# Kernel optimization log

Hardware: AMD Instinct MI355X
Metric: run time of the kernel (lower is better)

Reference implementation:

```python
import jax, jax.numpy as jnp
import numpy as np

B, D, M, P, I, O = 256, 10, 32, 36, 8, 16
NUM_ITERATIONS = 3
EPS = 1e-07


def squash(s, axis=-1):
    sq = jnp.sum(s * s, axis=axis, keepdims=True)
    safe_norm = jnp.sqrt(sq + EPS)
    scale = sq / (1.0 + sq)
    return scale * (s / safe_norm)


def setup_inputs() -> dict:
    key = jax.random.key(0)
    kx, kw = jax.random.split(key)
    x = jax.random.normal(kx, (B, M, P, I), dtype=jnp.float32)
    # Parameter shape matches torch: [1, D, M, 1, O, I]
    W = 0.01 * jax.random.normal(kw, (1, D, M, 1, O, I), dtype=jnp.float32)
    return {"x": x, "W": W}


def reference(x, W):
    Wd = W[0, :, :, 0]  # [D, M, O, I]
    # u_hat: [B, D, M, P, O]
    u_hat = jnp.einsum('dmoi,bmpi->bdmpo', Wd, x)
    tu = jax.lax.stop_gradient(u_hat)
    b = jnp.zeros(u_hat.shape[:4], dtype=u_hat.dtype)  # [B, D, M, P]
    for _ in range(NUM_ITERATIONS - 1):
        c = jax.nn.softmax(b, axis=1)                 # over digit caps
        s = jnp.einsum('bdmp,bdmpo->bdo', c, tu)
        v = squash(s)
        b = b + jnp.einsum('bdmpo,bdo->bdmp', tu, v)
    # Final softmax over dim=3 (primary-cap axis), faithful to source
    c = jax.nn.softmax(b, axis=3)
    s = jnp.einsum('bdmp,bdmpo->bdo', c, u_hat)
    return squash(s)
```

## Files before the change

kernel.cpp:

```cpp
#include <hip/hip_runtime.h>
#include <math.h>

#define BB 256
#define DD 10
#define MM 32
#define PP 36
#define II 8
#define OO 16
#define NT 320
#define XS 292
#define RS 37

__device__ __forceinline__ float dot8(const float4 a0, const float4 a1,
                                      const float4 b0, const float4 b1) {
    return a0.x*b0.x + a0.y*b0.y + a0.z*b0.z + a0.w*b0.w
         + a1.x*b1.x + a1.y*b1.y + a1.z*b1.z + a1.w*b1.w;
}
__device__ __forceinline__ float dot4(const float4 a, const float4 b) {
    return a.x*b.x + a.y*b.y + a.z*b.z + a.w*b.w;
}

__global__ void __launch_bounds__(NT, 3) caps_routing(
    const float* __restrict__ x,
    const float* __restrict__ W,
    float* __restrict__ out)
{
    const int bidx = blockIdx.x & 255;
    const int half = blockIdx.x >> 8;
    const int tid  = threadIdx.x;
    const int wave = tid >> 6;
    const int lane = tid & 63;
    const float* __restrict__ xb = x + (size_t)bidx * (MM*PP*II);

    __shared__ __align__(16) float xs  [MM*XS];
    __shared__ __align__(16) float z   [DD*MM*II];
    __shared__ __align__(16) float y   [5*MM*II];
    __shared__ __align__(16) float ybar[MM*II];
    __shared__ __align__(16) float rinv[MM*RS];

    {
        const float4* xg = (const float4*)xb;
        #pragma unroll
        for (int k = 0; k < 8; ++k) {
            const int t = tid + k*NT;
            if (t < MM*72) {
                const int m = t / 72, r = t - m*72;
                *(float4*)(xs + m*XS + 4*r) = xg[t];
            }
        }
        if (tid < MM*II) {
            const int m = tid >> 3, i = tid & 7;
            const float* xr = xb + m*(PP*II) + i;
            float acc = 0.f;
            #pragma unroll 6
            for (int p = 0; p < PP; ++p) acc += xr[p*II];
            ybar[tid] = 0.1f * acc;
        }
    }
    __syncthreads();

    {
        const int o = lane & 15, q = lane >> 4;
        #pragma unroll
        for (int r = 0; r < 2; ++r) {
            const int d = wave + r*5;
            float s1 = 0.f;
            #pragma unroll
            for (int j = 0; j < 8; ++j) {
                const int m = q*8 + j;
                const float4* wp = (const float4*)(W + ((size_t)((d*MM + m)*OO + o)) * II);
                const float4* yp = (const float4*)(ybar + m*II);
                s1 += dot8(wp[0], wp[1], yp[0], yp[1]);
            }
            s1 += __shfl_xor(s1, 16, 64);
            s1 += __shfl_xor(s1, 32, 64);
            float sq = s1 * s1;
            sq += __shfl_xor(sq, 1, 64);
            sq += __shfl_xor(sq, 2, 64);
            sq += __shfl_xor(sq, 4, 64);
            sq += __shfl_xor(sq, 8, 64);
            const float v1 = (sq / (1.f + sq)) * (s1 / sqrtf(sq + 1e-7f));
            float vv[OO];
            #pragma unroll
            for (int o2 = 0; o2 < OO; ++o2) vv[o2] = __shfl(v1, o2, 64);
            #pragma unroll
            for (int k = 0; k < 4; ++k) {
                const int mi = k*64 + lane;
                const int m = mi >> 3, i = mi & 7;
                const float* wp = W + ((size_t)(d*MM + m)*OO) * II + i;
                float acc = 0.f;
                #pragma unroll
                for (int o2 = 0; o2 < OO; ++o2) acc += wp[o2*II] * vv[o2];
                z[d*(MM*II) + mi] = acc;
            }
        }
    }
    __syncthreads();

    #pragma unroll
    for (int k = 0; k < 4; ++k) {
        const int t = tid + k*NT;
        if (t < MM*PP) {
            const int m = t / PP, p = t - m*PP;
            const float4* xp = (const float4*)(xs + m*XS + p*II);
            const float4 x0 = xp[0], x1 = xp[1];
            float se = 0.f;
            #pragma unroll
            for (int d2 = 0; d2 < DD; ++d2) {
                const float4* zp = (const float4*)(z + (d2*MM + m)*II);
                se += __expf(dot8(x0, x1, zp[0], zp[1]));
            }
            rinv[m*RS + p] = 1.0f / se;
        }
    }
    __syncthreads();

    {
        const int d = half*5 + wave;
        float* __restrict__ zd = z + d*(MM*II);
        float* __restrict__ yd = y + wave*(MM*II);

        const int mL = lane >> 1, ih = lane & 1;
        const float* xr = xs + mL*XS + ih*4;
        const float4 zh = *(const float4*)(zd + mL*II + ih*4);

        {
            const float* rr = rinv + mL*RS;
            float a0=0.f, a1=0.f, a2=0.f, a3=0.f;
            #pragma unroll 4
            for (int p = 0; p < PP; ++p) {
                const float4 xh = *(const float4*)(xr + p*II);
                float bh = dot4(xh, zh);
                bh += __shfl_xor(bh, 1, 64);
                const float e = __expf(bh) * rr[p];
                a0 += e*xh.x; a1 += e*xh.y; a2 += e*xh.z; a3 += e*xh.w;
            }
            *(float4*)(yd + mL*II + ih*4) = make_float4(a0,a1,a2,a3);
        }

        const int o = lane & 15, q = lane >> 4;
        float s2 = 0.f;
        #pragma unroll
        for (int j = 0; j < 8; ++j) {
            const int m = q*8 + j;
            const float4* wp = (const float4*)(W + ((size_t)((d*MM + m)*OO + o)) * II);
            const float4* yp = (const float4*)(yd + m*II);
            s2 += dot8(wp[0], wp[1], yp[0], yp[1]);
        }
        s2 += __shfl_xor(s2, 16, 64);
        s2 += __shfl_xor(s2, 32, 64);
        float sq = s2 * s2;
        sq += __shfl_xor(sq, 1, 64);
        sq += __shfl_xor(sq, 2, 64);
        sq += __shfl_xor(sq, 4, 64);
        sq += __shfl_xor(sq, 8, 64);
        const float v2 = (sq / (1.f + sq)) * (s2 / sqrtf(sq + 1e-7f));
        float vv[OO];
        #pragma unroll
        for (int o2 = 0; o2 < OO; ++o2) vv[o2] = __shfl(v2, o2, 64);

        #pragma unroll
        for (int k = 0; k < 4; ++k) {
            const int mi = k*64 + lane;
            const int m = mi >> 3, i = mi & 7;
            const float* wp = W + ((size_t)(d*MM + m)*OO) * II + i;
            float acc = 0.f;
            #pragma unroll
            for (int o2 = 0; o2 < OO; ++o2) acc += wp[o2*II] * vv[o2];
            zd[mi] += acc;
        }

        {
            const float4 zh2 = *(const float4*)(zd + mL*II + ih*4);
            float se = 0.f;
            float a0=0.f, a1=0.f, a2=0.f, a3=0.f;
            #pragma unroll 4
            for (int p = 0; p < PP; ++p) {
                const float4 xh = *(const float4*)(xr + p*II);
                float bh = dot4(xh, zh2);
                bh += __shfl_xor(bh, 1, 64);
                const float e = __expf(bh);
                se += e;
                a0 += e*xh.x; a1 += e*xh.y; a2 += e*xh.z; a3 += e*xh.w;
            }
            const float rs = 1.f / se;
            *(float4*)(yd + mL*II + ih*4) = make_float4(a0*rs, a1*rs, a2*rs, a3*rs);
        }

        float s3 = 0.f;
        #pragma unroll
        for (int j = 0; j < 8; ++j) {
            const int m = q*8 + j;
            const float4* wp = (const float4*)(W + ((size_t)((d*MM + m)*OO + o)) * II);
            const float4* yp = (const float4*)(yd + m*II);
            s3 += dot8(wp[0], wp[1], yp[0], yp[1]);
        }
        s3 += __shfl_xor(s3, 16, 64);
        s3 += __shfl_xor(s3, 32, 64);
        float sq3 = s3 * s3;
        sq3 += __shfl_xor(sq3, 1, 64);
        sq3 += __shfl_xor(sq3, 2, 64);
        sq3 += __shfl_xor(sq3, 4, 64);
        sq3 += __shfl_xor(sq3, 8, 64);
        const float r = (sq3 / (1.f + sq3)) * (s3 / sqrtf(sq3 + 1e-7f));
        if (lane < OO)
            out[(size_t)bidx * (DD*OO) + d*OO + o] = r;
    }
}

extern "C" void kernel_launch(void* const* d_in, const int* in_sizes, int n_in,
                              void* d_out, int out_size, void* d_ws, size_t ws_size,
                              hipStream_t stream) {
    (void)in_sizes; (void)n_in; (void)out_size; (void)d_ws; (void)ws_size;
    const float* x = (const float*)d_in[0];
    const float* W = (const float*)d_in[1];
    float* out = (float*)d_out;
    caps_routing<<<dim3(BB*2), dim3(NT), 0, stream>>>(x, W, out);
}
```

Measured before the change: 88.81 us.

## Use one 640-thread block per batch with one wave per digit capsule

Each block now handles a whole batch element, with 10 waves each owning one digit capsule. Before, two 320-thread blocks per batch each redundantly recomputed the first routing pass and the softmax denominators. The z update is rewritten so each lane computes a float4 slice with vectorized W loads and keeps the updated z in registers instead of reading it back from LDS. This halves the grid and removes the duplicated preamble work, but gives larger blocks with more LDS per block, which may lower occupancy (launch_bounds still requests 3 blocks).

```diff
diff --git a/kernel.cpp b/kernel.cpp
--- a/kernel.cpp
+++ b/kernel.cpp
@@ -7,7 +7,7 @@
 #define PP 36
 #define II 8
 #define OO 16
-#define NT 320
+#define NT 640
 #define XS 292
 #define RS 37
 
@@ -25,8 +25,7 @@
     const float* __restrict__ W,
     float* __restrict__ out)
 {
-    const int bidx = blockIdx.x & 255;
-    const int half = blockIdx.x >> 8;
+    const int bidx = blockIdx.x;
     const int tid  = threadIdx.x;
     const int wave = tid >> 6;
     const int lane = tid & 63;
@@ -34,14 +33,14 @@
 
     __shared__ __align__(16) float xs  [MM*XS];
     __shared__ __align__(16) float z   [DD*MM*II];
-    __shared__ __align__(16) float y   [5*MM*II];
+    __shared__ __align__(16) float y   [DD*MM*II];
     __shared__ __align__(16) float ybar[MM*II];
     __shared__ __align__(16) float rinv[MM*RS];
 
     {
         const float4* xg = (const float4*)xb;
         #pragma unroll
-        for (int k = 0; k < 8; ++k) {
+        for (int k = 0; k < 4; ++k) {
             const int t = tid + k*NT;
             if (t < MM*72) {
                 const int m = t / 72, r = t - m*72;
@@ -60,45 +59,43 @@
     __syncthreads();
 
     {
+        const int d = wave;
         const int o = lane & 15, q = lane >> 4;
-        #pragma unroll
-        for (int r = 0; r < 2; ++r) {
-            const int d = wave + r*5;
-            float s1 = 0.f;
-            #pragma unroll
-            for (int j = 0; j < 8; ++j) {
-                const int m = q*8 + j;
-                const float4* wp = (const float4*)(W + ((size_t)((d*MM + m)*OO + o)) * II);
-                const float4* yp = (const float4*)(ybar + m*II);
-                s1 += dot8(wp[0], wp[1], yp[0], yp[1]);
-            }
-            s1 += __shfl_xor(s1, 16, 64);
-            s1 += __shfl_xor(s1, 32, 64);
-            float sq = s1 * s1;
-            sq += __shfl_xor(sq, 1, 64);
-            sq += __shfl_xor(sq, 2, 64);
-            sq += __shfl_xor(sq, 4, 64);
-            sq += __shfl_xor(sq, 8, 64);
-            const float v1 = (sq / (1.f + sq)) * (s1 / sqrtf(sq + 1e-7f));
-            float vv[OO];
-            #pragma unroll
-            for (int o2 = 0; o2 < OO; ++o2) vv[o2] = __shfl(v1, o2, 64);
-            #pragma unroll
-            for (int k = 0; k < 4; ++k) {
-                const int mi = k*64 + lane;
-                const int m = mi >> 3, i = mi & 7;
-                const float* wp = W + ((size_t)(d*MM + m)*OO) * II + i;
-                float acc = 0.f;
-                #pragma unroll
-                for (int o2 = 0; o2 < OO; ++o2) acc += wp[o2*II] * vv[o2];
-                z[d*(MM*II) + mi] = acc;
-            }
-        }
+        float s1 = 0.f;
+        #pragma unroll
+        for (int j = 0; j < 8; ++j) {
+            const int m = q*8 + j;
+            const float4* wp = (const float4*)(W + ((size_t)((d*MM + m)*OO + o)) * II);
+            const float4* yp = (const float4*)(ybar + m*II);
+            s1 += dot8(wp[0], wp[1], yp[0], yp[1]);
+        }
+        s1 += __shfl_xor(s1, 16, 64);
+        s1 += __shfl_xor(s1, 32, 64);
+        float sq = s1 * s1;
+        sq += __shfl_xor(sq, 1, 64);
+        sq += __shfl_xor(sq, 2, 64);
+        sq += __shfl_xor(sq, 4, 64);
+        sq += __shfl_xor(sq, 8, 64);
+        const float v1 = (sq / (1.f + sq)) * (s1 / sqrtf(sq + 1e-7f));
+        float vv[OO];
+        #pragma unroll
+        for (int o2 = 0; o2 < OO; ++o2) vv[o2] = __shfl(v1, o2, 64);
+
+        const int mz = lane >> 1, ihz = lane & 1;
+        const float* wz = W + ((size_t)(d*MM + mz)*OO) * II + ihz*4;
+        float a0 = 0.f, a1 = 0.f, a2 = 0.f, a3 = 0.f;
+        #pragma unroll
+        for (int o2 = 0; o2 < OO; ++o2) {
+            const float4 wv = *(const float4*)(wz + o2*II);
+            a0 += wv.x * vv[o2]; a1 += wv.y * vv[o2];
+            a2 += wv.z * vv[o2]; a3 += wv.w * vv[o2];
+        }
+        *(float4*)(z + (d*MM + mz)*II + ihz*4) = make_float4(a0, a1, a2, a3);
     }
     __syncthreads();
 
     #pragma unroll
-    for (int k = 0; k < 4; ++k) {
+    for (int k = 0; k < 2; ++k) {
         const int t = tid + k*NT;
         if (t < MM*PP) {
             const int m = t / PP, p = t - m*PP;
@@ -116,9 +113,9 @@
     __syncthreads();
 
     {
-        const int d = half*5 + wave;
-        float* __restrict__ zd = z + d*(MM*II);
-        float* __restrict__ yd = y + wave*(MM*II);
+        const int d = wave;
+        const float* __restrict__ zd = z + d*(MM*II);
+        float* __restrict__ yd = y + d*(MM*II);
 
         const int mL = lane >> 1, ih = lane & 1;
         const float* xr = xs + mL*XS + ih*4;
@@ -127,7 +124,7 @@
         {
             const float* rr = rinv + mL*RS;
             float a0=0.f, a1=0.f, a2=0.f, a3=0.f;
-            #pragma unroll 4
+            #pragma unroll 6
             for (int p = 0; p < PP; ++p) {
                 const float4 xh = *(const float4*)(xr + p*II);
                 float bh = dot4(xh, zh);
@@ -159,22 +156,23 @@
         #pragma unroll
         for (int o2 = 0; o2 < OO; ++o2) vv[o2] = __shfl(v2, o2, 64);
 
-        #pragma unroll
-        for (int k = 0; k < 4; ++k) {
-            const int mi = k*64 + lane;
-            const int m = mi >> 3, i = mi & 7;
-            const float* wp = W + ((size_t)(d*MM + m)*OO) * II + i;
-            float acc = 0.f;
+        float4 zh2;
+        {
+            const float* wz = W + ((size_t)(d*MM + mL)*OO) * II + ih*4;
+            float a0 = 0.f, a1 = 0.f, a2 = 0.f, a3 = 0.f;
             #pragma unroll
-            for (int o2 = 0; o2 < OO; ++o2) acc += wp[o2*II] * vv[o2];
-            zd[mi] += acc;
+            for (int o2 = 0; o2 < OO; ++o2) {
+                const float4 wv = *(const float4*)(wz + o2*II);
+                a0 += wv.x * vv[o2]; a1 += wv.y * vv[o2];
+                a2 += wv.z * vv[o2]; a3 += wv.w * vv[o2];
+            }
+            zh2 = make_float4(zh.x + a0, zh.y + a1, zh.z + a2, zh.w + a3);
         }
 
         {
-            const float4 zh2 = *(const float4*)(zd + mL*II + ih*4);
             float se = 0.f;
             float a0=0.f, a1=0.f, a2=0.f, a3=0.f;
-            #pragma unroll 4
+            #pragma unroll 6
             for (int p = 0; p < PP; ++p) {
                 const float4 xh = *(const float4*)(xr + p*II);
                 float bh = dot4(xh, zh2);
@@ -215,5 +213,5 @@
     const float* x = (const float*)d_in[0];
     const float* W = (const float*)d_in[1];
     float* out = (float*)d_out;
-    caps_routing<<<dim3(BB*2), dim3(NT), 0, stream>>>(x, W, out);
-}
+    caps_routing<<<dim3(BB), dim3(NT), 0, stream>>>(x, W, out);
+}
```

After: 78.05 us. 12.1% less time.
